# Performance work log

Hardware: AMD Instinct MI355X
Metric: run time of the kernel (lower is better)

The kernel has to match this reference:

```python
import jax, jax.numpy as jnp
import numpy as np

N = 120000   # hits
K = 512      # non-noise objects (ids 1..K; id 0 = noise)
D = 8        # cluster-space dim
C = 6        # pid classes
Q_MIN = 1.0
NOISE_THR = 0
PAYLOAD_W = 1.0
EPS = 1e-9


def setup_inputs() -> dict:
    key = jax.random.key(0)
    ks = jax.random.split(key, 9)
    beta = jax.random.uniform(ks[0], (N,), dtype=jnp.float32) * 0.95 + 0.01  # keep arctanh finite
    x = jax.random.normal(ks[1], (N, D), dtype=jnp.float32)
    object_id = jax.random.randint(ks[2], (N,), 0, K + 1).astype(jnp.int32)
    # guarantee every object id (and noise id 0) appears at least once
    object_id = object_id.at[: K + 1].set(jnp.arange(K + 1, dtype=jnp.int32))
    energy = jax.random.normal(ks[3], (N,), dtype=jnp.float32)
    energy_per_hit = jax.random.normal(ks[4], (N,), dtype=jnp.float32)
    momentum = jax.random.normal(ks[5], (N, 3), dtype=jnp.float32)
    momentum_per_hit = jax.random.normal(ks[6], (N, 3), dtype=jnp.float32)
    pid_logits = jax.random.normal(ks[7], (N, C), dtype=jnp.float32)
    pid_per_hit = jax.random.randint(ks[8], (N,), 0, C).astype(jnp.int32)
    return dict(beta=beta, x=x, object_id=object_id, energy=energy,
                energy_per_hit=energy_per_hit, momentum=momentum,
                momentum_per_hit=momentum_per_hit, pid_logits=pid_logits,
                pid_per_hit=pid_per_hit)


def _oc_core(beta, x, object_id):
    """condensation_loss_tiger with weights=1, max_n_rep=0 (no repulsive sampling)."""
    oids = jnp.arange(1, K + 1, dtype=object_id.dtype)
    att_mask = object_id[:, None] == oids[None, :]              # [N, K]
    q = jnp.arctanh(beta) ** 2 + Q_MIN                          # [N]
    alphas = jnp.argmax(q[:, None] * att_mask, axis=0)          # [K] condensation points
    x_k = x[alphas]                                             # [K, D]
    q_k = q[alphas]                                             # [K]
    # squared euclidean distance via gemm (avoids [N,K,D] intermediate)
    d2 = (jnp.sum(x * x, axis=1)[:, None] + jnp.sum(x_k * x_k, axis=1)[None, :]
          - 2.0 * (x @ x_k.T))
    d2 = jnp.maximum(d2, 0.0)                                   # [N, K]
    dist = jnp.sqrt(jnp.maximum(d2, 1e-12))
    qw = q[:, None] * q_k[None, :]                              # [N, K]
    # attractive: per-object normalized by hits in object, then mean over objects
    att_norm = jnp.sum(att_mask, axis=0).astype(x.dtype)        # [K]
    v_att = jnp.sum(jnp.where(att_mask, qw * d2, 0.0) / (att_norm + EPS)[None, :]) / K
    # repulsive: hinge (1 - dist), normalized by n_hits not in object
    rep_mask = (~att_mask) & (dist < 1.0)
    n_rep_k = jnp.sum(~att_mask, axis=0).astype(x.dtype)        # [K]
    n_rep = jnp.sum(rep_mask)
    v_rep = jnp.sum(jnp.where(rep_mask, qw * (1.0 - dist), 0.0) / (n_rep_k + EPS)[None, :]) / K
    l_coward = jnp.mean(1.0 - beta[alphas])
    noise_m = (object_id <= NOISE_THR).astype(beta.dtype)
    l_noise = jnp.sum(beta * noise_m) / jnp.sum(noise_m)
    return v_att, v_rep, l_coward, l_noise, n_rep


def reference(beta, x, object_id, energy, energy_per_hit, momentum,
              momentum_per_hit, pid_logits, pid_per_hit):
    v_att, v_rep, l_coward, l_noise, n_rep = _oc_core(beta, x, object_id)
    oc_total = v_att + v_rep + l_coward + l_noise
    # payload losses on non-noise hits (masked means == F.*_loss on gathered rows)
    m = (object_id > NOISE_THR).astype(beta.dtype)              # [N]
    nm = jnp.sum(m)
    e_loss = jnp.sum((energy - energy_per_hit) ** 2 * m) / nm
    p_loss = jnp.sum((momentum - momentum_per_hit) ** 2 * m[:, None]) / (nm * momentum.shape[1])
    logp = jax.nn.log_softmax(pid_logits, axis=-1)              # [N, C]
    nll = -jnp.take_along_axis(logp, pid_per_hit[:, None], axis=1)[:, 0]
    pid_loss = jnp.sum(nll * m) / nm
    total = oc_total + PAYLOAD_W * (e_loss + p_loss + pid_loss)
    return (v_att, v_rep, l_coward, l_noise, n_rep.astype(jnp.float32),
            oc_total, e_loss, p_loss, pid_loss, total)
```

## Files before the change

kernel.cpp:

```cpp
#include <hip/hip_runtime.h>
#include <math.h>

#define KOBJ 512
#define KTW 8
#define TK 32
#define NTILE (KOBJ / TK)
#define HB 4
#define HCH (256 * HB)
#define MPREP 128

typedef _Float16 half2_t __attribute__((ext_vector_type(2)));

#define AGS(p, v) __hip_atomic_store((p), (v), __ATOMIC_RELAXED, __HIP_MEMORY_SCOPE_AGENT)
#define AGL(p)    __hip_atomic_load((p), __ATOMIC_RELAXED, __HIP_MEMORY_SCOPE_AGENT)

__device__ __forceinline__ float wave_red_f(float v) {
  #pragma unroll
  for (int off = 32; off > 0; off >>= 1) v += __shfl_down(v, off, 64);
  return v;
}

__device__ __forceinline__ float q_of_beta(float b) {
  float a = 0.5f * __logf((1.f + b) / (1.f - b));
  return fmaf(a, a, 1.f);
}

__device__ __forceinline__ float dot8h(uint4 kx, const uint* y, float acc) {
#if __has_builtin(__builtin_amdgcn_fdot2)
  acc = __builtin_amdgcn_fdot2(__builtin_bit_cast(half2_t, y[0]),
                               __builtin_bit_cast(half2_t, kx.x), acc, false);
  acc = __builtin_amdgcn_fdot2(__builtin_bit_cast(half2_t, y[1]),
                               __builtin_bit_cast(half2_t, kx.y), acc, false);
  acc = __builtin_amdgcn_fdot2(__builtin_bit_cast(half2_t, y[2]),
                               __builtin_bit_cast(half2_t, kx.z), acc, false);
  acc = __builtin_amdgcn_fdot2(__builtin_bit_cast(half2_t, y[3]),
                               __builtin_bit_cast(half2_t, kx.w), acc, false);
#else
  const uint kk[4] = {kx.x, kx.y, kx.z, kx.w};
  #pragma unroll
  for (int c = 0; c < 4; c++) {
    half2_t a = __builtin_bit_cast(half2_t, y[c]);
    half2_t b = __builtin_bit_cast(half2_t, kk[c]);
    acc = fmaf((float)a.x, (float)b.x, acc);
    acc = fmaf((float)a.y, (float)b.y, acc);
  }
#endif
  return acc;
}

__global__ __launch_bounds__(256) void
k_prep(const float* __restrict__ beta, const float* __restrict__ x,
       const int* __restrict__ oid,
       const float* __restrict__ energy, const float* __restrict__ eph,
       const float* __restrict__ mom, const float* __restrict__ mph,
       const float* __restrict__ logits, const int* __restrict__ pid,
       unsigned long long* __restrict__ amax_part,
       unsigned* __restrict__ cnt_part,
       float* __restrict__ scal_part,
       uint4* __restrict__ hry, uint4* __restrict__ hrm,
       unsigned* __restrict__ done_cnt, int n) {
  __shared__ unsigned long long lmax[KOBJ];
  __shared__ unsigned lcnt[KOBJ];
  if (blockIdx.x == 0 && threadIdx.x == 0) *done_cnt = 0u;
  for (int t = threadIdx.x; t < KOBJ; t += 256) { lmax[t] = 0ull; lcnt[t] = 0u; }
  __syncthreads();

  const float4* xp = (const float4*)x;
  float e_t = 0.f, p_t = 0.f, pid_t = 0.f, noise_t = 0.f, ncnt = 0.f, mcnt = 0.f;
  for (int i = blockIdx.x * 256 + threadIdx.x; i < n; i += MPREP * 256) {
    float b = beta[i];
    int o = oid[i];
    float q = q_of_beta(b);
    float4 xa = xp[2 * (size_t)i];
    float4 xb = xp[2 * (size_t)i + 1];
    float xi[8] = {xa.x, xa.y, xa.z, xa.w, xb.x, xb.y, xb.z, xb.w};
    float s = 0.f;
    #pragma unroll
    for (int c = 0; c < 8; c++) s = fmaf(xi[c], xi[c], s);
    uint4 r0;
    {
      half2_t h0 = { (_Float16)(-2.f * xi[0]), (_Float16)(-2.f * xi[1]) };
      half2_t h1 = { (_Float16)(-2.f * xi[2]), (_Float16)(-2.f * xi[3]) };
      half2_t h2 = { (_Float16)(-2.f * xi[4]), (_Float16)(-2.f * xi[5]) };
      half2_t h3 = { (_Float16)(-2.f * xi[6]), (_Float16)(-2.f * xi[7]) };
      r0.x = __builtin_bit_cast(uint, h0);
      r0.y = __builtin_bit_cast(uint, h1);
      r0.z = __builtin_bit_cast(uint, h2);
      r0.w = __builtin_bit_cast(uint, h3);
    }
    uint4 r1 = { __float_as_uint(s), __float_as_uint(q), (uint)o, 0u };
    hry[i] = r0;
    hrm[i] = r1;

    if (o > 0) {
      unsigned long long key = ((unsigned long long)__float_as_uint(q) << 32)
                             | (unsigned long long)(unsigned)(~(unsigned)i);
      atomicMax(&lmax[o - 1], key);
      atomicAdd(&lcnt[o - 1], 1u);
      mcnt += 1.f;
      float de = energy[i] - eph[i];
      e_t = fmaf(de, de, e_t);
      float p0 = mom[3*i+0] - mph[3*i+0];
      float p1 = mom[3*i+1] - mph[3*i+1];
      float p2 = mom[3*i+2] - mph[3*i+2];
      p_t = fmaf(p0, p0, p_t); p_t = fmaf(p1, p1, p_t); p_t = fmaf(p2, p2, p_t);
      const float* lg = logits + 6*i;
      float l0=lg[0], l1=lg[1], l2=lg[2], l3=lg[3], l4=lg[4], l5=lg[5];
      float mx = fmaxf(fmaxf(fmaxf(l0,l1),fmaxf(l2,l3)), fmaxf(l4,l5));
      float sm = __expf(l0-mx)+__expf(l1-mx)+__expf(l2-mx)
               + __expf(l3-mx)+__expf(l4-mx)+__expf(l5-mx);
      int pc = pid[i];
      float lp = (pc==0)?l0:(pc==1)?l1:(pc==2)?l2:(pc==3)?l3:(pc==4)?l4:l5;
      pid_t += mx + __logf(sm) - lp;
    } else {
      noise_t += b;
      ncnt += 1.f;
    }
  }
  __syncthreads();

  for (int t = threadIdx.x; t < KOBJ; t += 256) {
    amax_part[(size_t)blockIdx.x * KOBJ + t] = lmax[t];
    cnt_part[(size_t)blockIdx.x * KOBJ + t]  = lcnt[t];
  }

  float vals[6] = {e_t, p_t, pid_t, noise_t, ncnt, mcnt};
  #pragma unroll
  for (int j = 0; j < 6; j++) vals[j] = wave_red_f(vals[j]);
  __shared__ float sred[4][6];
  int w = threadIdx.x >> 6, l = threadIdx.x & 63;
  if (l == 0) {
    #pragma unroll
    for (int j = 0; j < 6; j++) sred[w][j] = vals[j];
  }
  __syncthreads();
  if (threadIdx.x == 0) {
    #pragma unroll
    for (int j = 0; j < 6; j++)
      scal_part[blockIdx.x * 8 + j] = sred[0][j]+sred[1][j]+sred[2][j]+sred[3][j];
  }
}

__global__ __launch_bounds__(256, 8) void
k_main(const float* __restrict__ x, const float* __restrict__ beta,
       const uint4* __restrict__ hry, const uint4* __restrict__ hrm,
       const unsigned long long* __restrict__ amax_part,
       const unsigned* __restrict__ cnt_part,
       const float* __restrict__ scal_part,
       float* __restrict__ cow_part, float* __restrict__ pairs_part,
       unsigned* __restrict__ done_cnt, float* __restrict__ out, int n) {
  __shared__ __align__(16) uint skt[(TK + 1) * KTW];
  __shared__ unsigned long long skey[8][32];
  __shared__ unsigned scnt_s[8][32];
  __shared__ float sredu[4][10];
  __shared__ unsigned slast;

  const int tid = threadIdx.x;
  const int w = tid >> 6, l = tid & 63;
  const int tile0 = blockIdx.y * TK;
  const int hbase = blockIdx.x * HCH;
  const int nblk = gridDim.x * gridDim.y;
  const int bid = blockIdx.y * gridDim.x + blockIdx.x;

  {
    int ko = tid & 31, seg = tid >> 5;
    unsigned long long key = 0ull;
    unsigned cnt = 0u;
    for (int m = seg; m < MPREP; m += 8) {
      unsigned long long km = amax_part[(size_t)m * KOBJ + tile0 + ko];
      key = (km > key) ? km : key;
      cnt += cnt_part[(size_t)m * KOBJ + tile0 + ko];
    }
    skey[seg][ko] = key;
    scnt_s[seg][ko] = cnt;
    __syncthreads();
    float cowv = 0.f;
    if (tid < 32) {
      #pragma unroll
      for (int c = 1; c < 8; c++) {
        unsigned long long kc = skey[c][tid];
        key = (kc > key) ? kc : key;
        cnt += scnt_s[c][tid];
      }
      unsigned idx = ~(unsigned)(key & 0xffffffffull);
      float q_k = __uint_as_float((unsigned)(key >> 32));
      const float4* xp4 = (const float4*)x;
      float4 xa = xp4[2 * (size_t)idx];
      float4 xb = xp4[2 * (size_t)idx + 1];
      float xv[8] = {xa.x, xa.y, xa.z, xa.w, xb.x, xb.y, xb.z, xb.w};
      float s2 = 0.f;
      #pragma unroll
      for (int c = 0; c < 8; c++) s2 = fmaf(xv[c], xv[c], s2);
      uint* kt = &skt[tid * KTW];
      #pragma unroll
      for (int c = 0; c < 4; c++) {
        half2_t hp = { (_Float16)xv[2*c], (_Float16)xv[2*c+1] };
        kt[c] = __builtin_bit_cast(uint, hp);
      }
      kt[4] = __float_as_uint(s2);
      kt[5] = __float_as_uint(q_k / ((float)(n - (int)cnt) + 1e-9f));
      kt[6] = __float_as_uint(q_k / ((float)cnt + 1e-9f));
      kt[7] = 0u;
      if (blockIdx.x == 0) cowv = 1.f - beta[idx];
    }
    if (tid < 8) skt[TK * KTW + tid] = 0u;
    if (tid < 64) {
      cowv = wave_red_f(cowv);
      if (tid == 0 && blockIdx.x == 0) AGS(&cow_part[blockIdx.y], cowv);
    }
    __syncthreads();
  }

  uint yh[HB][4];
  float thr[HB], bh2[HB], qi[HB];
  int own[HB];
  #pragma unroll
  for (int h = 0; h < HB; h++) {
    int i = hbase + h * 256 + tid;
    if (i < n) {
      uint4 ra = hry[i];
      uint4 rb = hrm[i];
      yh[h][0] = ra.x; yh[h][1] = ra.y; yh[h][2] = ra.z; yh[h][3] = ra.w;
      float s = __uint_as_float(rb.x);
      bh2[h] = s;
      thr[h] = 1.f - s;
      qi[h] = __uint_as_float(rb.y);
      own[h] = (int)rb.z - 1 - tile0;
    } else {
      #pragma unroll
      for (int c = 0; c < 4; c++) yh[h][c] = 0u;
      bh2[h] = 0.f;
      thr[h] = -1e30f;
      qi[h] = 0.f;
      own[h] = -1;
    }
  }

  float att = 0.f, rep = 0.f, nrep = 0.f;
  const uint4* skt4 = (const uint4*)skt;
  uint4 kxa = skt4[0], kxb = skt4[1];
  #pragma unroll 2
  for (int k2 = 0; k2 < TK; k2++) {
    uint4 nxa = skt4[2 * k2 + 2];
    uint4 nxb = skt4[2 * k2 + 3];
    float s2 = __uint_as_float(kxb.x);
    float wr = __uint_as_float(kxb.y);
    #pragma unroll
    for (int h = 0; h < HB; h++) {
      float dp = dot8h(kxa, yh[h], s2);
      if (dp < thr[h]) {
        float d2 = dp + bh2[h];
        float dist = sqrtf(fmaxf(d2, 1e-12f));
        rep = fmaf(qi[h] * (1.f - dist), wr, rep);
        nrep += 1.f;
      }
    }
    kxa = nxa; kxb = nxb;
  }

  #pragma unroll
  for (int h = 0; h < HB; h++) {
    int ko = own[h];
    if (ko >= 0 && ko < TK) {
      uint4 ka = skt4[2 * ko];
      uint4 kb = skt4[2 * ko + 1];
      float s2 = __uint_as_float(kb.x);
      float wr = __uint_as_float(kb.y);
      float wa = __uint_as_float(kb.z);
      float dp = dot8h(ka, yh[h], s2);
      float d2 = dp + bh2[h];
      att = fmaf(qi[h] * fmaxf(d2, 0.f), wa, att);
      if (dp < thr[h]) {
        float dist = sqrtf(fmaxf(d2, 1e-12f));
        rep = fmaf(-qi[h] * (1.f - dist), wr, rep);
        nrep -= 1.f;
      }
    }
  }

  att = wave_red_f(att);
  rep = wave_red_f(rep);
  nrep = wave_red_f(nrep);
  if (l == 0) { sredu[w][0] = att; sredu[w][1] = rep; sredu[w][2] = nrep; }
  __syncthreads();
  if (tid == 0) {
    AGS(&pairs_part[bid * 4 + 0], sredu[0][0]+sredu[1][0]+sredu[2][0]+sredu[3][0]);
    AGS(&pairs_part[bid * 4 + 1], sredu[0][1]+sredu[1][1]+sredu[2][1]+sredu[3][1]);
    AGS(&pairs_part[bid * 4 + 2], sredu[0][2]+sredu[1][2]+sredu[2][2]+sredu[3][2]);
    slast = __hip_atomic_fetch_add(done_cnt, 1u, __ATOMIC_ACQ_REL,
                                   __HIP_MEMORY_SCOPE_AGENT);
  }
  __syncthreads();

  if (slast == (unsigned)(nblk - 1)) {
    float v[10] = {0,0,0,0,0,0,0,0,0,0};
    for (int b2 = tid; b2 < nblk; b2 += 256) {
      v[0] += AGL(&pairs_part[b2 * 4 + 0]);
      v[1] += AGL(&pairs_part[b2 * 4 + 1]);
      v[2] += AGL(&pairs_part[b2 * 4 + 2]);
    }
    for (int m = tid; m < MPREP; m += 256) {
      #pragma unroll
      for (int j = 0; j < 6; j++) v[3 + j] += scal_part[m * 8 + j];
    }
    for (int g = tid; g < NTILE; g += 256) v[9] += AGL(&cow_part[g]);
    #pragma unroll
    for (int j = 0; j < 10; j++) v[j] = wave_red_f(v[j]);
    __syncthreads();
    if (l == 0) {
      #pragma unroll
      for (int j = 0; j < 10; j++) sredu[w][j] = v[j];
    }
    __syncthreads();
    if (tid == 0) {
      float t10[10];
      #pragma unroll
      for (int j = 0; j < 10; j++)
        t10[j] = sredu[0][j]+sredu[1][j]+sredu[2][j]+sredu[3][j];
      float v_att  = t10[0] / (float)KOBJ;
      float v_rep  = t10[1] / (float)KOBJ;
      float n_rep  = t10[2];
      float l_cow  = t10[9] / (float)KOBJ;
      float l_noise = t10[6] / t10[7];
      float oc = v_att + v_rep + l_cow + l_noise;
      float nm = t10[8];
      float e_loss  = t10[3] / nm;
      float p_loss  = t10[4] / (nm * 3.f);
      float pid_loss = t10[5] / nm;
      out[0] = v_att;
      out[1] = v_rep;
      out[2] = l_cow;
      out[3] = l_noise;
      out[4] = n_rep;
      out[5] = oc;
      out[6] = e_loss;
      out[7] = p_loss;
      out[8] = pid_loss;
      out[9] = oc + e_loss + p_loss + pid_loss;
    }
  }
}

extern "C" void kernel_launch(void* const* d_in, const int* in_sizes, int n_in,
                              void* d_out, int out_size, void* d_ws, size_t ws_size,
                              hipStream_t stream) {
  const float* beta   = (const float*)d_in[0];
  const float* x      = (const float*)d_in[1];
  const int*   oid    = (const int*)d_in[2];
  const float* energy = (const float*)d_in[3];
  const float* eph    = (const float*)d_in[4];
  const float* mom    = (const float*)d_in[5];
  const float* mph    = (const float*)d_in[6];
  const float* logits = (const float*)d_in[7];
  const int*   pid    = (const int*)d_in[8];
  float* outp = (float*)d_out;
  const int n = in_sizes[0];
  const int nhb = (n + HCH - 1) / HCH;
  const int nblk_tot = nhb * NTILE;

  char* base = (char*)d_ws;
  size_t off = 0;
  float* cow_part   = (float*)(base + off); off += (size_t)NTILE * 4;
  float* pairs_part = (float*)(base + off); off += (size_t)nblk_tot * 4 * 4;
  float* scal_part  = (float*)(base + off); off += (size_t)MPREP * 8 * 4;
  unsigned* done_cnt = (unsigned*)(base + off); off += 256;
  off = (off + 255) & ~(size_t)255;
  unsigned long long* amax_part = (unsigned long long*)(base + off); off += (size_t)MPREP * KOBJ * 8;
  unsigned* cnt_part = (unsigned*)(base + off);                      off += (size_t)MPREP * KOBJ * 4;
  off = (off + 255) & ~(size_t)255;
  uint4* hry = (uint4*)(base + off); off += (size_t)(nhb * HCH) * 16;
  uint4* hrm = (uint4*)(base + off); off += (size_t)(nhb * HCH) * 16;

  k_prep<<<MPREP, 256, 0, stream>>>(beta, x, oid, energy, eph, mom, mph, logits, pid,
                                    amax_part, cnt_part, scal_part, hry, hrm,
                                    done_cnt, n);
  k_main<<<dim3(nhb, NTILE), 256, 0, stream>>>(x, beta, hry, hrm, amax_part, cnt_part,
                                               scal_part, cow_part, pairs_part,
                                               done_cnt, outp, n);
}
```

Baseline: 133.6 us.

## Split condensation-point gather into separate kernel and retile pair loop

Adds a separate gather kernel that reduces the per-object argmax and count partials once and writes a global object table, instead of every main block redoing that reduction. The pair kernel now holds one hit per thread and walks 128 objects per tile, reading object data straight from global/L1 rather than LDS, and k_prep now uses 256 partial blocks. This removes the redundant per-block prep work at the cost of an extra kernel launch, lower per-thread reuse of the object data, and more blocks in the grid.

```diff
diff --git a/kernel.cpp b/kernel.cpp
--- a/kernel.cpp
+++ b/kernel.cpp
@@ -3,11 +3,10 @@
 
 #define KOBJ 512
 #define KTW 8
-#define TK 32
-#define NTILE (KOBJ / TK)
-#define HB 4
-#define HCH (256 * HB)
-#define MPREP 128
+#define TKP 128
+#define NTILEP (KOBJ / TKP)
+#define MPREP 256
+#define GB 64
 
 typedef _Float16 half2_t __attribute__((ext_vector_type(2)));
 
@@ -141,140 +140,146 @@
   }
 }
 
-__global__ __launch_bounds__(256, 8) void
-k_main(const float* __restrict__ x, const float* __restrict__ beta,
-       const uint4* __restrict__ hry, const uint4* __restrict__ hrm,
-       const unsigned long long* __restrict__ amax_part,
-       const unsigned* __restrict__ cnt_part,
-       const float* __restrict__ scal_part,
-       float* __restrict__ cow_part, float* __restrict__ pairs_part,
-       unsigned* __restrict__ done_cnt, float* __restrict__ out, int n) {
-  __shared__ __align__(16) uint skt[(TK + 1) * KTW];
-  __shared__ unsigned long long skey[8][32];
-  __shared__ unsigned scnt_s[8][32];
+__global__ __launch_bounds__(256) void
+k_gather(const float* __restrict__ x, const float* __restrict__ beta,
+         const unsigned long long* __restrict__ amax_part,
+         const unsigned* __restrict__ cnt_part,
+         uint* __restrict__ ktab, float* __restrict__ cow_part, int n) {
+  __shared__ unsigned long long skey[32][8];
+  __shared__ unsigned scnt[32][8];
+  const int o = threadIdx.x & 7, seg = threadIdx.x >> 3;
+  const int k = blockIdx.x * 8 + o;
+
+  unsigned long long key = 0ull;
+  unsigned cnt = 0u;
+  for (int m = seg; m < MPREP; m += 32) {
+    unsigned long long km = amax_part[(size_t)m * KOBJ + k];
+    key = (km > key) ? km : key;
+    cnt += cnt_part[(size_t)m * KOBJ + k];
+  }
+  skey[seg][o] = key;
+  scnt[seg][o] = cnt;
+  __syncthreads();
+  for (int s = 16; s > 0; s >>= 1) {
+    if (seg < s) {
+      unsigned long long k2 = skey[seg + s][o];
+      if (k2 > skey[seg][o]) skey[seg][o] = k2;
+      scnt[seg][o] += scnt[seg + s][o];
+    }
+    __syncthreads();
+  }
+
+  float cowv = 0.f;
+  if (threadIdx.x < 8) {
+    key = skey[0][o];
+    cnt = scnt[0][o];
+    unsigned idx = ~(unsigned)(key & 0xffffffffull);
+    float q_k = __uint_as_float((unsigned)(key >> 32));
+    const float4* xp = (const float4*)x;
+    float4 xa = xp[2 * (size_t)idx];
+    float4 xb = xp[2 * (size_t)idx + 1];
+    float xv[8] = {xa.x, xa.y, xa.z, xa.w, xb.x, xb.y, xb.z, xb.w};
+    float s2 = 0.f;
+    #pragma unroll
+    for (int c = 0; c < 8; c++) s2 = fmaf(xv[c], xv[c], s2);
+    uint* kt = ktab + (size_t)k * KTW;
+    #pragma unroll
+    for (int c = 0; c < 4; c++) {
+      half2_t hp = { (_Float16)xv[2*c], (_Float16)xv[2*c+1] };
+      kt[c] = __builtin_bit_cast(uint, hp);
+    }
+    kt[4] = __float_as_uint(s2);
+    kt[5] = __float_as_uint(q_k / ((float)(n - (int)cnt) + 1e-9f));
+    kt[6] = __float_as_uint(q_k / ((float)cnt + 1e-9f));
+    kt[7] = 0u;
+    cowv = 1.f - beta[idx];
+  }
+  if (threadIdx.x < 64) {
+    cowv = wave_red_f(cowv);
+    if (threadIdx.x == 0) cow_part[blockIdx.x] = cowv;
+  }
+  if (blockIdx.x == 0 && threadIdx.x >= 64 && threadIdx.x < 80)
+    ktab[(size_t)KOBJ * KTW + (threadIdx.x - 64)] = 0u;
+}
+
+__global__ __launch_bounds__(256, 4) void
+k_pairs(const uint4* __restrict__ hry, const uint4* __restrict__ hrm,
+        const uint* __restrict__ ktab,
+        const float* __restrict__ scal_part, const float* __restrict__ cow_part,
+        float* __restrict__ pairs_part, unsigned* __restrict__ done_cnt,
+        float* __restrict__ out, int n) {
   __shared__ float sredu[4][10];
   __shared__ unsigned slast;
-
   const int tid = threadIdx.x;
   const int w = tid >> 6, l = tid & 63;
-  const int tile0 = blockIdx.y * TK;
-  const int hbase = blockIdx.x * HCH;
+  const int tile0 = blockIdx.y * TKP;
+  const int i = blockIdx.x * 256 + tid;
   const int nblk = gridDim.x * gridDim.y;
   const int bid = blockIdx.y * gridDim.x + blockIdx.x;
 
-  {
-    int ko = tid & 31, seg = tid >> 5;
-    unsigned long long key = 0ull;
-    unsigned cnt = 0u;
-    for (int m = seg; m < MPREP; m += 8) {
-      unsigned long long km = amax_part[(size_t)m * KOBJ + tile0 + ko];
-      key = (km > key) ? km : key;
-      cnt += cnt_part[(size_t)m * KOBJ + tile0 + ko];
-    }
-    skey[seg][ko] = key;
-    scnt_s[seg][ko] = cnt;
-    __syncthreads();
-    float cowv = 0.f;
-    if (tid < 32) {
-      #pragma unroll
-      for (int c = 1; c < 8; c++) {
-        unsigned long long kc = skey[c][tid];
-        key = (kc > key) ? kc : key;
-        cnt += scnt_s[c][tid];
-      }
-      unsigned idx = ~(unsigned)(key & 0xffffffffull);
-      float q_k = __uint_as_float((unsigned)(key >> 32));
-      const float4* xp4 = (const float4*)x;
-      float4 xa = xp4[2 * (size_t)idx];
-      float4 xb = xp4[2 * (size_t)idx + 1];
-      float xv[8] = {xa.x, xa.y, xa.z, xa.w, xb.x, xb.y, xb.z, xb.w};
-      float s2 = 0.f;
-      #pragma unroll
-      for (int c = 0; c < 8; c++) s2 = fmaf(xv[c], xv[c], s2);
-      uint* kt = &skt[tid * KTW];
-      #pragma unroll
-      for (int c = 0; c < 4; c++) {
-        half2_t hp = { (_Float16)xv[2*c], (_Float16)xv[2*c+1] };
-        kt[c] = __builtin_bit_cast(uint, hp);
-      }
-      kt[4] = __float_as_uint(s2);
-      kt[5] = __float_as_uint(q_k / ((float)(n - (int)cnt) + 1e-9f));
-      kt[6] = __float_as_uint(q_k / ((float)cnt + 1e-9f));
-      kt[7] = 0u;
-      if (blockIdx.x == 0) cowv = 1.f - beta[idx];
-    }
-    if (tid < 8) skt[TK * KTW + tid] = 0u;
-    if (tid < 64) {
-      cowv = wave_red_f(cowv);
-      if (tid == 0 && blockIdx.x == 0) AGS(&cow_part[blockIdx.y], cowv);
-    }
-    __syncthreads();
-  }
-
-  uint yh[HB][4];
-  float thr[HB], bh2[HB], qi[HB];
-  int own[HB];
-  #pragma unroll
-  for (int h = 0; h < HB; h++) {
-    int i = hbase + h * 256 + tid;
-    if (i < n) {
-      uint4 ra = hry[i];
-      uint4 rb = hrm[i];
-      yh[h][0] = ra.x; yh[h][1] = ra.y; yh[h][2] = ra.z; yh[h][3] = ra.w;
-      float s = __uint_as_float(rb.x);
-      bh2[h] = s;
-      thr[h] = 1.f - s;
-      qi[h] = __uint_as_float(rb.y);
-      own[h] = (int)rb.z - 1 - tile0;
-    } else {
-      #pragma unroll
-      for (int c = 0; c < 4; c++) yh[h][c] = 0u;
-      bh2[h] = 0.f;
-      thr[h] = -1e30f;
-      qi[h] = 0.f;
-      own[h] = -1;
-    }
-  }
-
+  uint yh[4];
+  float thr, bh, qi;
+  int own;
+  if (i < n) {
+    uint4 ra = hry[i];
+    uint4 rb = hrm[i];
+    yh[0] = ra.x; yh[1] = ra.y; yh[2] = ra.z; yh[3] = ra.w;
+    float s = __uint_as_float(rb.x);
+    bh = s;
+    thr = 1.f - s;
+    qi = __uint_as_float(rb.y);
+    own = (int)rb.z - 1 - tile0;
+  } else {
+    yh[0] = yh[1] = yh[2] = yh[3] = 0u;
+    bh = 0.f; thr = -1e30f; qi = 0.f; own = -1;
+  }
+
+  const uint4* kt4 = (const uint4*)ktab + (size_t)tile0 * 2;
   float att = 0.f, rep = 0.f, nrep = 0.f;
-  const uint4* skt4 = (const uint4*)skt;
-  uint4 kxa = skt4[0], kxb = skt4[1];
+  uint4 a0 = kt4[0], b0 = kt4[1];
+  uint4 a1 = kt4[2], b1 = kt4[3];
   #pragma unroll 2
-  for (int k2 = 0; k2 < TK; k2++) {
-    uint4 nxa = skt4[2 * k2 + 2];
-    uint4 nxb = skt4[2 * k2 + 3];
-    float s2 = __uint_as_float(kxb.x);
-    float wr = __uint_as_float(kxb.y);
-    #pragma unroll
-    for (int h = 0; h < HB; h++) {
-      float dp = dot8h(kxa, yh[h], s2);
-      if (dp < thr[h]) {
-        float d2 = dp + bh2[h];
+  for (int r = 0; r < TKP; r += 2) {
+    uint4 na0 = kt4[2*r + 4], nb0 = kt4[2*r + 5];
+    uint4 na1 = kt4[2*r + 6], nb1 = kt4[2*r + 7];
+    {
+      float s2 = __uint_as_float(b0.x);
+      float wr = __uint_as_float(b0.y);
+      float dp = dot8h(a0, yh, s2);
+      if (dp < thr) {
+        float d2 = dp + bh;
         float dist = sqrtf(fmaxf(d2, 1e-12f));
-        rep = fmaf(qi[h] * (1.f - dist), wr, rep);
+        rep = fmaf(qi * (1.f - dist), wr, rep);
         nrep += 1.f;
       }
     }
-    kxa = nxa; kxb = nxb;
-  }
-
-  #pragma unroll
-  for (int h = 0; h < HB; h++) {
-    int ko = own[h];
-    if (ko >= 0 && ko < TK) {
-      uint4 ka = skt4[2 * ko];
-      uint4 kb = skt4[2 * ko + 1];
-      float s2 = __uint_as_float(kb.x);
-      float wr = __uint_as_float(kb.y);
-      float wa = __uint_as_float(kb.z);
-      float dp = dot8h(ka, yh[h], s2);
-      float d2 = dp + bh2[h];
-      att = fmaf(qi[h] * fmaxf(d2, 0.f), wa, att);
-      if (dp < thr[h]) {
+    {
+      float s2 = __uint_as_float(b1.x);
+      float wr = __uint_as_float(b1.y);
+      float dp = dot8h(a1, yh, s2);
+      if (dp < thr) {
+        float d2 = dp + bh;
         float dist = sqrtf(fmaxf(d2, 1e-12f));
-        rep = fmaf(-qi[h] * (1.f - dist), wr, rep);
-        nrep -= 1.f;
+        rep = fmaf(qi * (1.f - dist), wr, rep);
+        nrep += 1.f;
       }
+    }
+    a0 = na0; b0 = nb0; a1 = na1; b1 = nb1;
+  }
+
+  if (own >= 0 && own < TKP) {
+    uint4 ka = kt4[2*own];
+    uint4 kb = kt4[2*own + 1];
+    float s2 = __uint_as_float(kb.x);
+    float wr = __uint_as_float(kb.y);
+    float wa = __uint_as_float(kb.z);
+    float dp = dot8h(ka, yh, s2);
+    float d2 = dp + bh;
+    att = fmaf(qi * fmaxf(d2, 0.f), wa, att);
+    if (dp < thr) {
+      float dist = sqrtf(fmaxf(d2, 1e-12f));
+      rep = fmaf(-qi * (1.f - dist), wr, rep);
+      nrep -= 1.f;
     }
   }
 
@@ -303,7 +308,7 @@
       #pragma unroll
       for (int j = 0; j < 6; j++) v[3 + j] += scal_part[m * 8 + j];
     }
-    for (int g = tid; g < NTILE; g += 256) v[9] += AGL(&cow_part[g]);
+    for (int g = tid; g < GB; g += 256) v[9] += cow_part[g];
     #pragma unroll
     for (int j = 0; j < 10; j++) v[j] = wave_red_f(v[j]);
     __syncthreads();
@@ -355,12 +360,13 @@
   const int*   pid    = (const int*)d_in[8];
   float* outp = (float*)d_out;
   const int n = in_sizes[0];
-  const int nhb = (n + HCH - 1) / HCH;
-  const int nblk_tot = nhb * NTILE;
+  const int nch = (n + 255) / 256;
+  const int nblk_tot = nch * NTILEP;
 
   char* base = (char*)d_ws;
   size_t off = 0;
-  float* cow_part   = (float*)(base + off); off += (size_t)NTILE * 4;
+  uint*  ktab       = (uint*)(base + off);  off += (size_t)(KOBJ + 2) * KTW * 4;
+  float* cow_part   = (float*)(base + off); off += (size_t)GB * 4;
   float* pairs_part = (float*)(base + off); off += (size_t)nblk_tot * 4 * 4;
   float* scal_part  = (float*)(base + off); off += (size_t)MPREP * 8 * 4;
   unsigned* done_cnt = (unsigned*)(base + off); off += 256;
@@ -368,13 +374,13 @@
   unsigned long long* amax_part = (unsigned long long*)(base + off); off += (size_t)MPREP * KOBJ * 8;
   unsigned* cnt_part = (unsigned*)(base + off);                      off += (size_t)MPREP * KOBJ * 4;
   off = (off + 255) & ~(size_t)255;
-  uint4* hry = (uint4*)(base + off); off += (size_t)(nhb * HCH) * 16;
-  uint4* hrm = (uint4*)(base + off); off += (size_t)(nhb * HCH) * 16;
+  uint4* hry = (uint4*)(base + off); off += (size_t)nch * 256 * 16;
+  uint4* hrm = (uint4*)(base + off); off += (size_t)nch * 256 * 16;
 
   k_prep<<<MPREP, 256, 0, stream>>>(beta, x, oid, energy, eph, mom, mph, logits, pid,
                                     amax_part, cnt_part, scal_part, hry, hrm,
                                     done_cnt, n);
-  k_main<<<dim3(nhb, NTILE), 256, 0, stream>>>(x, beta, hry, hrm, amax_part, cnt_part,
-                                               scal_part, cow_part, pairs_part,
-                                               done_cnt, outp, n);
-}
+  k_gather<<<GB, 256, 0, stream>>>(x, beta, amax_part, cnt_part, ktab, cow_part, n);
+  k_pairs<<<dim3(nch, NTILEP), 256, 0, stream>>>(hry, hrm, ktab, scal_part, cow_part,
+                                                 pairs_part, done_cnt, outp, n);
+}
```

Result: slower. 141.4 us (+5.8%).
